# Kernel optimization log

Measured on AMD Instinct MI355X. Metric: run time of the kernel, lower is better.

Reference implementation:

```python
import jax, jax.numpy as jnp
import numpy as np

N = 16384   # total queries (= total keys here)
B = 16      # scenes
K = 1024    # keys per scene (key_batch_cnt entries)
L = 32      # local neighborhood size
D = 256     # d_model
H = 8       # nhead
DFF = 1024
LN_EPS = 1e-5


def setup_inputs() -> dict:
    key = jax.random.key(0)
    ks = jax.random.split(key, 32)
    f32 = jnp.float32

    def lin(k, o, i):
        return jax.random.normal(k, (o, i), f32) * 0.02

    idx = jax.random.randint(ks[3], (N, L), 0, K)
    invalid = jax.random.uniform(ks[4], (N, L)) < 0.1
    index_pair = jnp.where(invalid, -1, idx).astype(jnp.int32)

    inp = {
        "tgt": jax.random.normal(ks[0], (N, D), f32),
        "memory": jax.random.normal(ks[1], (N, D), f32),
        "memory_pos_emb": jax.random.normal(ks[2], (N, D), f32),
        "key_batch_cnt": jnp.full((B,), K, dtype=jnp.int32),
        "index_pair": index_pair,
        "index_pair_batch": jnp.repeat(jnp.arange(B, dtype=jnp.int32), K),
        "Wq": lin(ks[5], D, D), "bq": jnp.zeros((D,), f32),
        "Wkc": lin(ks[6], D, D), "bkc": jnp.zeros((D,), f32),
        "Wkp": lin(ks[7], D, D), "bkp": jnp.zeros((D,), f32),
        "Wv": lin(ks[8], D, D), "bv": jnp.zeros((D,), f32),
        "Wo": lin(ks[9], D, D), "bo": jnp.zeros((D,), f32),
        "W1": lin(ks[10], DFF, D), "b1": jnp.zeros((DFF,), f32),
        "W2": lin(ks[11], D, DFF), "b2": jnp.zeros((D,), f32),
        "g2": jnp.ones((D,), f32), "be2": jnp.zeros((D,), f32),
        "g3": jnp.ones((D,), f32), "be3": jnp.zeros((D,), f32),
    }
    return inp


def _ln(x, g, b):
    m = jnp.mean(x, axis=-1, keepdims=True)
    v = jnp.mean((x - m) ** 2, axis=-1, keepdims=True)
    return (x - m) * jax.lax.rsqrt(v + LN_EPS) * g + b


def reference(tgt, memory, memory_pos_emb, key_batch_cnt, index_pair,
              index_pair_batch, Wq, bq, Wkc, bkc, Wkp, bkp, Wv, bv,
              Wo, bo, W1, b1, W2, b2, g2, be2, g3, be3):
    Dh = D // H
    scale = Dh ** -0.5

    # dense projections
    q = tgt @ Wq.T + bq                              # [N, D]
    k = (memory @ Wkc.T + bkc) + (memory_pos_emb @ Wkp.T + bkp)  # content + pos
    v = memory @ Wv.T + bv

    # local-index gather: per-batch indices -> global key indices
    offsets = jnp.concatenate([jnp.zeros((1,), jnp.int32),
                               jnp.cumsum(key_batch_cnt)[:-1].astype(jnp.int32)])
    mask = index_pair < 0                            # [N, L] padded neighbors
    gidx = jnp.where(mask, 0, index_pair + offsets[index_pair_batch][:, None])

    kg = k[gidx].reshape(N, L, H, Dh)                # gathered keys  [N,L,H,Dh]
    vg = v[gidx].reshape(N, L, H, Dh)                # gathered values
    qh = q.reshape(N, H, Dh)

    attn = jnp.einsum('nhd,nlhd->nhl', qh, kg) * scale
    attn = jnp.where(mask[:, None, :], -1e9, attn)
    attn = jax.nn.softmax(attn, axis=-1)
    out = jnp.einsum('nhl,nlhd->nhd', attn, vg).reshape(N, D)
    tgt2 = out @ Wo.T + bo                           # attention out_proj

    x = _ln(tgt + tgt2, g2, be2)
    ff = jax.nn.relu(x @ W1.T + b1) @ W2.T + b2
    return _ln(x + ff, g3, be3)
```

## Files before the change

### kernel.cpp

```cpp
#include <hip/hip_runtime.h>
#include <stdint.h>

#define N_TOT 16384
#define LNEI  32
#define DM    256
#define NH    8
#define DH    32
#define DFF   1024

typedef __attribute__((ext_vector_type(8))) short  short8;
typedef __attribute__((ext_vector_type(4))) float  floatx4;
typedef __attribute__((ext_vector_type(4))) unsigned short ushort4_t;
typedef __attribute__((ext_vector_type(4))) unsigned int uint4_t;

static __device__ __forceinline__ float b2f(unsigned short u) {
  union { unsigned int u; float f; } x; x.u = ((unsigned int)u) << 16; return x.f;
}
static __device__ __forceinline__ unsigned short f2b(float f) {
  union { float f; unsigned int u; } x; x.f = f;
  unsigned int r = x.u + 0x7fffu + ((x.u >> 16) & 1u);
  return (unsigned short)(r >> 16);
}
static __device__ __forceinline__ float lo16(unsigned int d) {
  union { unsigned int u; float f; } x; x.u = d << 16; return x.f;
}
static __device__ __forceinline__ float hi16(unsigned int d) {
  union { unsigned int u; float f; } x; x.u = d & 0xffff0000u; return x.f;
}

#define NSEG 11
struct Seg { const float* src; unsigned short* dst; int cols; int ostride; int ooff; int begin; };
struct SegTable { Seg s[NSEG]; int total; };

__global__ __launch_bounds__(256) void cvt_all(SegTable T, float* biaskv,
                                               const float* bkc, const float* bkp,
                                               const float* bv) {
  int e = (blockIdx.x * 256 + threadIdx.x) * 4;
  if (e >= T.total) {
    int c = e - T.total;
    #pragma unroll
    for (int j = 0; j < 4; ++j, ++c)
      if (c < 512) biaskv[c] = (c < 256) ? (bkc[c] + bkp[c]) : bv[c - 256];
    return;
  }
  int si = 0;
  #pragma unroll
  for (int i = 1; i < NSEG; ++i) if (e >= T.s[i].begin) si = i;
  const Seg s = T.s[si];
  const int le = e - s.begin;
  const int row = le / s.cols;
  const int col = le - row * s.cols;
  floatx4 v = {0.f, 0.f, 0.f, 0.f};
  if (s.src) v = *(const floatx4*)(s.src + le);
  ushort4_t o;
  o.x = f2b(v[0]); o.y = f2b(v[1]); o.z = f2b(v[2]); o.w = f2b(v[3]);
  *(ushort4_t*)(s.dst + (size_t)row * s.ostride + s.ooff + col) = o;
}

static __device__ __forceinline__ void gl_lds16(const unsigned short* g, unsigned short* l) {
  __builtin_amdgcn_global_load_lds(
      (const __attribute__((address_space(1))) unsigned int*)g,
      (__attribute__((address_space(3))) unsigned int*)l, 16, 0, 0);
}

template<bool RELU>
__global__ __launch_bounds__(64) void gemm_w1(
    const unsigned short* __restrict__ A, const unsigned short* __restrict__ W,
    const float* __restrict__ bias,
    unsigned short* __restrict__ C, int M, int Nd, int K, int lda)
{
  constexpr int BK = 32;
  __shared__ unsigned short sA[2][32 * BK];
  __shared__ unsigned short sB[2][64 * BK];

  const int lane = threadIdx.x;
  const int quad = lane >> 4;
  const int l16  = lane & 15;
  const int m0 = blockIdx.x * 32;
  const int n0 = blockIdx.y * 64;

  const int srow = lane >> 2;
  const int scol = (lane & 3) * 8;

  floatx4 acc[2][4] = {};

  for (int k0 = 0; k0 < K; k0 += 2 * BK) {
    __syncthreads();
    #pragma unroll
    for (int half = 0; half < 2; ++half) {
      const int kk = k0 + half * BK;
      #pragma unroll
      for (int c = 0; c < 2; ++c)
        gl_lds16(A + (size_t)(m0 + c * 16 + srow) * lda + kk + scol, &sA[half][c * 512]);
      #pragma unroll
      for (int c = 0; c < 4; ++c)
        gl_lds16(W + (size_t)(n0 + c * 16 + srow) * K + kk + scol, &sB[half][c * 512]);
    }
    __syncthreads();

    #pragma unroll
    for (int half = 0; half < 2; ++half) {
      short8 af[2], bf[4];
      #pragma unroll
      for (int mi = 0; mi < 2; ++mi)
        af[mi] = *(const short8*)&sA[half][(mi * 16 + l16) * BK + quad * 8];
      #pragma unroll
      for (int ni = 0; ni < 4; ++ni)
        bf[ni] = *(const short8*)&sB[half][(ni * 16 + l16) * BK + quad * 8];
      #pragma unroll
      for (int mi = 0; mi < 2; ++mi)
        #pragma unroll
        for (int ni = 0; ni < 4; ++ni)
          acc[mi][ni] = __builtin_amdgcn_mfma_f32_16x16x32_bf16(af[mi], bf[ni], acc[mi][ni], 0, 0, 0);
    }
  }

  #pragma unroll
  for (int ni = 0; ni < 4; ++ni) {
    const int col = n0 + ni * 16 + l16;
    const float bvv = bias[col];
    #pragma unroll
    for (int mi = 0; mi < 2; ++mi) {
      const int row0 = m0 + mi * 16 + quad * 4;
      #pragma unroll
      for (int i = 0; i < 4; ++i) {
        float v = acc[mi][ni][i] + bvv;
        if (RELU) v = fmaxf(v, 0.f);
        C[(size_t)(row0 + i) * Nd + col] = f2b(v);
      }
    }
  }
}

template<int BN, bool RELU>
__global__ __launch_bounds__(256) void gemm_tile(
    const unsigned short* __restrict__ A, const unsigned short* __restrict__ W,
    const float* __restrict__ bias,
    unsigned short* __restrict__ C, int M, int Nd, int K, int lda)
{
  constexpr int BM = 128, BK = 32;
  constexpr int MI = 4, NI = 4;
  __shared__ unsigned short sA[2][BM * BK];
  __shared__ unsigned short sB[2][BN * BK];

  const int w    = threadIdx.x >> 6;
  const int lane = threadIdx.x & 63;
  const int quad = lane >> 4;
  const int l16  = lane & 15;
  const int m0 = blockIdx.x * BM;
  const int n0 = blockIdx.y * BN;
  const int wrow0 = (w >> 1) * 64;
  const int wcol0 = (w & 1) * 64;

  const int aflat0 = w * 512 + lane * 8;
  const int ar0 = aflat0 >> 5, ac = aflat0 & 31;

  floatx4 acc[MI][NI] = {};

  for (int k0 = 0; k0 < K; k0 += 2 * BK) {
    __syncthreads();
    #pragma unroll
    for (int half = 0; half < 2; ++half) {
      const int kk = k0 + half * BK;
      #pragma unroll
      for (int c = 0; c < 2; ++c) {
        const int row = ar0 + c * 64;
        gl_lds16(A + (size_t)(m0 + row) * lda + kk + ac, &sA[half][(c * 4 + w) * 512]);
        gl_lds16(W + (size_t)(n0 + row) * K + kk + ac, &sB[half][(c * 4 + w) * 512]);
      }
    }
    __syncthreads();

    #pragma unroll
    for (int half = 0; half < 2; ++half) {
      short8 af[MI], bf[NI];
      #pragma unroll
      for (int mi = 0; mi < MI; ++mi)
        af[mi] = *(const short8*)&sA[half][(wrow0 + mi * 16 + l16) * BK + quad * 8];
      #pragma unroll
      for (int ni = 0; ni < NI; ++ni)
        bf[ni] = *(const short8*)&sB[half][(wcol0 + ni * 16 + l16) * BK + quad * 8];
      #pragma unroll
      for (int mi = 0; mi < MI; ++mi)
        #pragma unroll
        for (int ni = 0; ni < NI; ++ni)
          acc[mi][ni] = __builtin_amdgcn_mfma_f32_16x16x32_bf16(af[mi], bf[ni], acc[mi][ni], 0, 0, 0);
    }
  }

  #pragma unroll
  for (int ni = 0; ni < NI; ++ni) {
    const int col = n0 + wcol0 + ni * 16 + l16;
    const float bvv = bias[col];
    #pragma unroll
    for (int mi = 0; mi < MI; ++mi) {
      const int row0 = m0 + wrow0 + mi * 16 + quad * 4;
      #pragma unroll
      for (int i = 0; i < 4; ++i) {
        float v = acc[mi][ni][i] + bvv;
        if (RELU) v = fmaxf(v, 0.f);
        C[(size_t)(row0 + i) * Nd + col] = f2b(v);
      }
    }
  }
}

__global__ __launch_bounds__(256) void attn_kernel(
    const unsigned short* __restrict__ q, const unsigned short* __restrict__ kv,
    const int* __restrict__ key_batch_cnt, const int* __restrict__ index_pair,
    const int* __restrict__ index_pair_batch,
    unsigned short* __restrict__ out)
{
  const int n = ((blockIdx.x & 7) << 11) | (blockIdx.x >> 3);
  const int t = threadIdx.x;
  __shared__ float s_q[DM];
  __shared__ int   s_gidx[LNEI];
  __shared__ float s_prob[NH][LNEI];
  __shared__ float s_out[2][DM];

  s_q[t] = b2f(q[(size_t)n * DM + t]);
  if (t < LNEI) {
    const int b = index_pair_batch[n];
    int off = 0;
    for (int i = 0; i < b; ++i) off += key_batch_cnt[i];
    const int ip = index_pair[(size_t)n * LNEI + t];
    s_gidx[t] = (ip < 0) ? -1 : (ip + off);
  }
  __syncthreads();

  {
    const int h = t >> 5;
    const int l = t & 31;
    const int g = s_gidx[l];

    floatx4 qv[8];
    #pragma unroll
    for (int c = 0; c < 8; ++c) qv[c] = *(const floatx4*)&s_q[h * DH + c * 4];

    float score = -1e9f;
    if (g >= 0) {
      const uint4_t* kp = (const uint4_t*)(kv + (size_t)g * 512 + h * DH);
      float acc = 0.f;
      #pragma unroll
      for (int c = 0; c < 4; ++c) {
        uint4_t d = kp[c];
        acc += lo16(d.x) * qv[c * 2][0] + hi16(d.x) * qv[c * 2][1]
             + lo16(d.y) * qv[c * 2][2] + hi16(d.y) * qv[c * 2][3]
             + lo16(d.z) * qv[c * 2 + 1][0] + hi16(d.z) * qv[c * 2 + 1][1]
             + lo16(d.w) * qv[c * 2 + 1][2] + hi16(d.w) * qv[c * 2 + 1][3];
      }
      score = acc * 0.17677669529663687f;
    }

    float mx = score;
    #pragma unroll
    for (int msk = 16; msk >= 1; msk >>= 1) mx = fmaxf(mx, __shfl_xor(mx, msk, 64));
    const float e = __expf(score - mx);
    float sm = e;
    #pragma unroll
    for (int msk = 16; msk >= 1; msk >>= 1) sm += __shfl_xor(sm, msk, 64);
    s_prob[h][l] = e / sm;
  }
  __syncthreads();

  {
    const int jh  = t >> 7;
    const int h   = (t >> 4) & 7;
    const int dh2 = t & 15;
    float ax = 0.f, ay = 0.f;
    const unsigned short* vbase = kv + 256 + h * DH + dh2 * 2;
    #pragma unroll
    for (int j2 = 0; j2 < 16; ++j2) {
      const int j = jh * 16 + j2;
      int gj = s_gidx[j];
      gj = (gj < 0) ? 0 : gj;
      const float p = s_prob[h][j];
      const unsigned int d = *(const unsigned int*)(vbase + (size_t)gj * 512);
      ax += p * lo16(d);
      ay += p * hi16(d);
    }
    s_out[jh][h * DH + dh2 * 2]     = ax;
    s_out[jh][h * DH + dh2 * 2 + 1] = ay;
  }
  __syncthreads();

  out[(size_t)n * DM + t] = f2b(s_out[0][t] + s_out[1][t]);
}

template<bool IN1F32, bool OUTF32>
__global__ __launch_bounds__(256) void ln_kernel(
    const void* __restrict__ in1, const unsigned short* __restrict__ in2,
    const float* __restrict__ g, const float* __restrict__ b,
    void* __restrict__ out)
{
  const int n = blockIdx.x;
  const int t = threadIdx.x;
  const int wv = t >> 6;
  __shared__ float part[8];

  float a1;
  if (IN1F32) a1 = ((const float*)in1)[(size_t)n * DM + t];
  else        a1 = b2f(((const unsigned short*)in1)[(size_t)n * DM + t]);
  const float a = a1 + b2f(in2[(size_t)n * DM + t]);

  float s = a;
  #pragma unroll
  for (int msk = 32; msk >= 1; msk >>= 1) s += __shfl_xor(s, msk, 64);
  if ((t & 63) == 0) part[wv] = s;
  __syncthreads();
  const float mean = (part[0] + part[1] + part[2] + part[3]) * (1.0f / DM);
  const float d = a - mean;
  float s2 = d * d;
  #pragma unroll
  for (int msk = 32; msk >= 1; msk >>= 1) s2 += __shfl_xor(s2, msk, 64);
  if ((t & 63) == 0) part[4 + wv] = s2;
  __syncthreads();
  const float var = (part[4] + part[5] + part[6] + part[7]) * (1.0f / DM);
  const float y = d * rsqrtf(var + 1e-5f) * g[t] + b[t];
  if (OUTF32) ((float*)out)[(size_t)n * DM + t] = y;
  else        ((unsigned short*)out)[(size_t)n * DM + t] = f2b(y);
}

extern "C" void kernel_launch(void* const* d_in, const int* in_sizes, int n_in,
                              void* d_out, int out_size, void* d_ws, size_t ws_size,
                              hipStream_t stream) {
  const float* tgt  = (const float*)d_in[0];
  const float* mem  = (const float*)d_in[1];
  const float* pos  = (const float*)d_in[2];
  const int* kbc    = (const int*)d_in[3];
  const int* ipair  = (const int*)d_in[4];
  const int* ipb    = (const int*)d_in[5];
  const float* Wq   = (const float*)d_in[6];
  const float* bq   = (const float*)d_in[7];
  const float* Wkc  = (const float*)d_in[8];
  const float* bkc  = (const float*)d_in[9];
  const float* Wkp  = (const float*)d_in[10];
  const float* bkp  = (const float*)d_in[11];
  const float* Wv   = (const float*)d_in[12];
  const float* bvp  = (const float*)d_in[13];
  const float* Wo   = (const float*)d_in[14];
  const float* bo   = (const float*)d_in[15];
  const float* W1   = (const float*)d_in[16];
  const float* b1   = (const float*)d_in[17];
  const float* W2   = (const float*)d_in[18];
  const float* b2   = (const float*)d_in[19];
  const float* g2   = (const float*)d_in[20];
  const float* be2  = (const float*)d_in[21];
  const float* g3   = (const float*)d_in[22];
  const float* be3  = (const float*)d_in[23];

  const size_t NB = (size_t)N_TOT * DM;
  unsigned short* ws = (unsigned short*)d_ws;
  unsigned short* tgt_b = ws;
  unsigned short* ao_b  = ws;
  unsigned short* t2_b  = ws + NB;
  unsigned short* mp_b  = ws + 2 * NB;
  unsigned short* x_b   = ws + 2 * NB;
  unsigned short* ff_b  = ws + 3 * NB;
  unsigned short* q_b   = ws + 4 * NB;
  unsigned short* h1_b  = ws + 4 * NB;
  unsigned short* kv_b  = ws + 5 * NB;
  unsigned short* wgt   = ws + 8 * NB;
  unsigned short* Wq_b  = wgt;
  unsigned short* Wkv_b = wgt + 65536;
  unsigned short* Wo_b  = wgt + 65536 + 262144;
  unsigned short* W1_b  = wgt + 2 * 65536 + 262144;
  unsigned short* W2_b  = wgt + 2 * 65536 + 2 * 262144;
  float* bias_kv = (float*)(wgt + 2 * 65536 + 3 * 262144);

  SegTable T;
  int beg = 0, i = 0;
  auto seg = [&](const float* s, unsigned short* d, int cols, int ostride, int ooff, int nelem) {
    T.s[i].src = s; T.s[i].dst = d; T.s[i].cols = cols;
    T.s[i].ostride = ostride; T.s[i].ooff = ooff; T.s[i].begin = beg;
    beg += nelem; ++i;
  };
  seg(tgt, tgt_b, DM, DM, 0,   (int)NB);
  seg(mem, mp_b,  DM, 512, 0,  (int)NB);
  seg(pos, mp_b,  DM, 512, DM, (int)NB);
  seg(Wq,  Wq_b,  DM, DM, 0,   65536);
  seg(Wkc, Wkv_b, DM, 512, 0,  65536);
  seg(Wkp, Wkv_b, DM, 512, DM, 65536);
  seg(Wv,  Wkv_b + (size_t)256 * 512, DM, 512, 0, 65536);
  seg(nullptr, Wkv_b + (size_t)256 * 512, DM, 512, DM, 65536);
  seg(Wo,  Wo_b,  DM, DM, 0,   65536);
  seg(W1,  W1_b,  DM, DM, 0,   262144);
  seg(W2,  W2_b,  DFF, DFF, 0, 262144);
  T.total = beg;

  dim3 blk(256);
  cvt_all<<<dim3(T.total / 1024 + 1), blk, 0, stream>>>(T, bias_kv, bkc, bkp, bvp);

  dim3 blk64(64);
  dim3 gQ(N_TOT / 32, DM / 64);
  dim3 gKV(N_TOT / 32, 512 / 64);
  dim3 gF(N_TOT / 128, DFF / 128);

  gemm_w1<false><<<gQ, blk64, 0, stream>>>(tgt_b, Wq_b, bq, q_b, N_TOT, DM, DM, DM);
  gemm_w1<false><<<gKV, blk64, 0, stream>>>(mp_b, Wkv_b, bias_kv, kv_b, N_TOT, 512, 512, 512);
  attn_kernel<<<dim3(N_TOT), blk, 0, stream>>>(q_b, kv_b, kbc, ipair, ipb, ao_b);
  gemm_w1<false><<<gQ, blk64, 0, stream>>>(ao_b, Wo_b, bo, t2_b, N_TOT, DM, DM, DM);
  ln_kernel<true, false><<<dim3(N_TOT), blk, 0, stream>>>(tgt, t2_b, g2, be2, x_b);
  gemm_tile<128, true><<<gF, blk, 0, stream>>>(x_b, W1_b, b1, h1_b, N_TOT, DFF, DM, DM);
  gemm_w1<false><<<gQ, blk64, 0, stream>>>(h1_b, W2_b, b2, ff_b, N_TOT, DM, DFF, DFF);
  ln_kernel<false, true><<<dim3(N_TOT), blk, 0, stream>>>(x_b, ff_b, g3, be3, d_out);
}
```

Baseline: 291.9 us.

## Merge Q/KV GEMMs, retile small GEMMs, precompute batch offsets, restructure attention

Q and KV projections now run as one launch with 128x64 tiles over four waves, replacing the single-wave 32x64 blocks. The Wo and W2 GEMMs switch to 512-thread 128x64 tiles, and W1 uses a cleaned-up 128x128 tile. The conversion kernel computes scene offsets once, so each attention block no longer loops over key_batch_cnt. Attention now splits score computation across (neighbor, head) threads through shared memory and writes output through split x/y buffers. The goals are more work per block, less launch overhead and less redundant per-query work, at the cost of fewer blocks in flight and extra shared-memory passes.

```diff
diff --git a/kernel.cpp b/kernel.cpp
--- a/kernel.cpp
+++ b/kernel.cpp
@@ -34,10 +34,17 @@
 
 __global__ __launch_bounds__(256) void cvt_all(SegTable T, float* biaskv,
                                                const float* bkc, const float* bkp,
-                                               const float* bv) {
+                                               const float* bv,
+                                               int* offs, const int* kbc) {
   int e = (blockIdx.x * 256 + threadIdx.x) * 4;
   if (e >= T.total) {
     int c = e - T.total;
+    if (c == 512) {
+      int off = 0;
+      #pragma unroll
+      for (int i = 0; i < 16; ++i) { offs[i] = off; off += kbc[i]; }
+      return;
+    }
     #pragma unroll
     for (int j = 0; j < 4; ++j, ++c)
       if (c < 512) biaskv[c] = (c < 256) ? (bkc[c] + bkp[c]) : bv[c - 256];
@@ -63,38 +70,33 @@
       (__attribute__((address_space(3))) unsigned int*)l, 16, 0, 0);
 }
 
-template<bool RELU>
-__global__ __launch_bounds__(64) void gemm_w1(
+__device__ __forceinline__ void gemm4_body(
     const unsigned short* __restrict__ A, const unsigned short* __restrict__ W,
-    const float* __restrict__ bias,
-    unsigned short* __restrict__ C, int M, int Nd, int K, int lda)
-{
-  constexpr int BK = 32;
-  __shared__ unsigned short sA[2][32 * BK];
-  __shared__ unsigned short sB[2][64 * BK];
-
-  const int lane = threadIdx.x;
+    const float* __restrict__ bias, unsigned short* __restrict__ C,
+    int Nd, int K, int lda, int mb, int nb,
+    unsigned short (&sA)[2][4096], unsigned short (&sB)[2][2048])
+{
+  const int w    = threadIdx.x >> 6;
+  const int lane = threadIdx.x & 63;
   const int quad = lane >> 4;
   const int l16  = lane & 15;
-  const int m0 = blockIdx.x * 32;
-  const int n0 = blockIdx.y * 64;
-
-  const int srow = lane >> 2;
-  const int scol = (lane & 3) * 8;
+  const int m0 = mb * 128;
+  const int n0 = nb * 64;
+  const int wrow0 = w * 32;
+  const int aflat0 = w * 512 + lane * 8;
+  const int ar0 = aflat0 >> 5, ac = aflat0 & 31;
 
   floatx4 acc[2][4] = {};
 
-  for (int k0 = 0; k0 < K; k0 += 2 * BK) {
-    __syncthreads();
-    #pragma unroll
-    for (int half = 0; half < 2; ++half) {
-      const int kk = k0 + half * BK;
+  for (int k0 = 0; k0 < K; k0 += 64) {
+    __syncthreads();
+    #pragma unroll
+    for (int half = 0; half < 2; ++half) {
+      const int kk = k0 + half * 32;
       #pragma unroll
       for (int c = 0; c < 2; ++c)
-        gl_lds16(A + (size_t)(m0 + c * 16 + srow) * lda + kk + scol, &sA[half][c * 512]);
-      #pragma unroll
-      for (int c = 0; c < 4; ++c)
-        gl_lds16(W + (size_t)(n0 + c * 16 + srow) * K + kk + scol, &sB[half][c * 512]);
+        gl_lds16(A + (size_t)(m0 + ar0 + c * 64) * lda + kk + ac, &sA[half][(c * 4 + w) * 512]);
+      gl_lds16(W + (size_t)(n0 + ar0) * K + kk + ac, &sB[half][w * 512]);
     }
     __syncthreads();
 
@@ -103,10 +105,10 @@
       short8 af[2], bf[4];
       #pragma unroll
       for (int mi = 0; mi < 2; ++mi)
-        af[mi] = *(const short8*)&sA[half][(mi * 16 + l16) * BK + quad * 8];
+        af[mi] = *(const short8*)&sA[half][(wrow0 + mi * 16 + l16) * 32 + quad * 8];
       #pragma unroll
       for (int ni = 0; ni < 4; ++ni)
-        bf[ni] = *(const short8*)&sB[half][(ni * 16 + l16) * BK + quad * 8];
+        bf[ni] = *(const short8*)&sB[half][(ni * 16 + l16) * 32 + quad * 8];
       #pragma unroll
       for (int mi = 0; mi < 2; ++mi)
         #pragma unroll
@@ -121,7 +123,145 @@
     const float bvv = bias[col];
     #pragma unroll
     for (int mi = 0; mi < 2; ++mi) {
-      const int row0 = m0 + mi * 16 + quad * 4;
+      const int row0 = m0 + wrow0 + mi * 16 + quad * 4;
+      #pragma unroll
+      for (int i = 0; i < 4; ++i)
+        C[(size_t)(row0 + i) * Nd + col] = f2b(acc[mi][ni][i] + bvv);
+    }
+  }
+}
+
+__global__ __launch_bounds__(256) void gemm_qkv(
+    const unsigned short* __restrict__ A1, const unsigned short* __restrict__ W1p,
+    const float* __restrict__ b1p, unsigned short* __restrict__ C1,
+    const unsigned short* __restrict__ A2, const unsigned short* __restrict__ W2p,
+    const float* __restrict__ b2p, unsigned short* __restrict__ C2)
+{
+  __shared__ unsigned short sA[2][4096];
+  __shared__ unsigned short sB[2][2048];
+  const int bid = blockIdx.x;
+  if (bid < 512) {
+    gemm4_body(A1, W1p, b1p, C1, 256, 256, 256, bid >> 2, bid & 3, sA, sB);
+  } else {
+    const int b2 = bid - 512;
+    gemm4_body(A2, W2p, b2p, C2, 512, 512, 512, b2 >> 3, b2 & 7, sA, sB);
+  }
+}
+
+template<bool RELU>
+__global__ __launch_bounds__(512) void gemm8(
+    const unsigned short* __restrict__ A, const unsigned short* __restrict__ W,
+    const float* __restrict__ bias, unsigned short* __restrict__ C,
+    int Nd, int K, int lda)
+{
+  __shared__ unsigned short sA[2][4096];
+  __shared__ unsigned short sB[2][2048];
+  const int w    = threadIdx.x >> 6;
+  const int lane = threadIdx.x & 63;
+  const int quad = lane >> 4;
+  const int l16  = lane & 15;
+  const int m0 = blockIdx.x * 128;
+  const int n0 = blockIdx.y * 64;
+  const int srow = lane >> 2;
+  const int scol = (lane & 3) * 8;
+
+  floatx4 acc[4] = {};
+
+  for (int k0 = 0; k0 < K; k0 += 64) {
+    __syncthreads();
+    #pragma unroll
+    for (int half = 0; half < 2; ++half) {
+      const int kk = k0 + half * 32;
+      gl_lds16(A + (size_t)(m0 + w * 16 + srow) * lda + kk + scol, &sA[half][w * 512]);
+      if (w < 4)
+        gl_lds16(W + (size_t)(n0 + w * 16 + srow) * K + kk + scol, &sB[half][w * 512]);
+    }
+    __syncthreads();
+
+    #pragma unroll
+    for (int half = 0; half < 2; ++half) {
+      short8 af = *(const short8*)&sA[half][(w * 16 + l16) * 32 + quad * 8];
+      #pragma unroll
+      for (int ni = 0; ni < 4; ++ni) {
+        short8 bf = *(const short8*)&sB[half][(ni * 16 + l16) * 32 + quad * 8];
+        acc[ni] = __builtin_amdgcn_mfma_f32_16x16x32_bf16(af, bf, acc[ni], 0, 0, 0);
+      }
+    }
+  }
+
+  #pragma unroll
+  for (int ni = 0; ni < 4; ++ni) {
+    const int col = n0 + ni * 16 + l16;
+    const float bvv = bias[col];
+    const int row0 = m0 + w * 16 + quad * 4;
+    #pragma unroll
+    for (int i = 0; i < 4; ++i) {
+      float v = acc[ni][i] + bvv;
+      if (RELU) v = fmaxf(v, 0.f);
+      C[(size_t)(row0 + i) * Nd + col] = f2b(v);
+    }
+  }
+}
+
+template<bool RELU>
+__global__ __launch_bounds__(256) void gemm_tile128(
+    const unsigned short* __restrict__ A, const unsigned short* __restrict__ W,
+    const float* __restrict__ bias, unsigned short* __restrict__ C,
+    int Nd, int K, int lda)
+{
+  __shared__ unsigned short sA[2][4096];
+  __shared__ unsigned short sB[2][4096];
+  const int w    = threadIdx.x >> 6;
+  const int lane = threadIdx.x & 63;
+  const int quad = lane >> 4;
+  const int l16  = lane & 15;
+  const int m0 = blockIdx.x * 128;
+  const int n0 = blockIdx.y * 128;
+  const int wrow0 = (w >> 1) * 64;
+  const int wcol0 = (w & 1) * 64;
+  const int aflat0 = w * 512 + lane * 8;
+  const int ar0 = aflat0 >> 5, ac = aflat0 & 31;
+
+  floatx4 acc[4][4] = {};
+
+  for (int k0 = 0; k0 < K; k0 += 64) {
+    __syncthreads();
+    #pragma unroll
+    for (int half = 0; half < 2; ++half) {
+      const int kk = k0 + half * 32;
+      #pragma unroll
+      for (int c = 0; c < 2; ++c) {
+        const int row = ar0 + c * 64;
+        gl_lds16(A + (size_t)(m0 + row) * lda + kk + ac, &sA[half][(c * 4 + w) * 512]);
+        gl_lds16(W + (size_t)(n0 + row) * K + kk + ac, &sB[half][(c * 4 + w) * 512]);
+      }
+    }
+    __syncthreads();
+
+    #pragma unroll
+    for (int half = 0; half < 2; ++half) {
+      short8 af[4], bf[4];
+      #pragma unroll
+      for (int mi = 0; mi < 4; ++mi)
+        af[mi] = *(const short8*)&sA[half][(wrow0 + mi * 16 + l16) * 32 + quad * 8];
+      #pragma unroll
+      for (int ni = 0; ni < 4; ++ni)
+        bf[ni] = *(const short8*)&sB[half][(wcol0 + ni * 16 + l16) * 32 + quad * 8];
+      #pragma unroll
+      for (int mi = 0; mi < 4; ++mi)
+        #pragma unroll
+        for (int ni = 0; ni < 4; ++ni)
+          acc[mi][ni] = __builtin_amdgcn_mfma_f32_16x16x32_bf16(af[mi], bf[ni], acc[mi][ni], 0, 0, 0);
+    }
+  }
+
+  #pragma unroll
+  for (int ni = 0; ni < 4; ++ni) {
+    const int col = n0 + wcol0 + ni * 16 + l16;
+    const float bvv = bias[col];
+    #pragma unroll
+    for (int mi = 0; mi < 4; ++mi) {
+      const int row0 = m0 + wrow0 + mi * 16 + quad * 4;
       #pragma unroll
       for (int i = 0; i < 4; ++i) {
         float v = acc[mi][ni][i] + bvv;
@@ -132,130 +272,57 @@
   }
 }
 
-template<int BN, bool RELU>
-__global__ __launch_bounds__(256) void gemm_tile(
-    const unsigned short* __restrict__ A, const unsigned short* __restrict__ W,
-    const float* __restrict__ bias,
-    unsigned short* __restrict__ C, int M, int Nd, int K, int lda)
-{
-  constexpr int BM = 128, BK = 32;
-  constexpr int MI = 4, NI = 4;
-  __shared__ unsigned short sA[2][BM * BK];
-  __shared__ unsigned short sB[2][BN * BK];
-
-  const int w    = threadIdx.x >> 6;
-  const int lane = threadIdx.x & 63;
-  const int quad = lane >> 4;
-  const int l16  = lane & 15;
-  const int m0 = blockIdx.x * BM;
-  const int n0 = blockIdx.y * BN;
-  const int wrow0 = (w >> 1) * 64;
-  const int wcol0 = (w & 1) * 64;
-
-  const int aflat0 = w * 512 + lane * 8;
-  const int ar0 = aflat0 >> 5, ac = aflat0 & 31;
-
-  floatx4 acc[MI][NI] = {};
-
-  for (int k0 = 0; k0 < K; k0 += 2 * BK) {
-    __syncthreads();
-    #pragma unroll
-    for (int half = 0; half < 2; ++half) {
-      const int kk = k0 + half * BK;
-      #pragma unroll
-      for (int c = 0; c < 2; ++c) {
-        const int row = ar0 + c * 64;
-        gl_lds16(A + (size_t)(m0 + row) * lda + kk + ac, &sA[half][(c * 4 + w) * 512]);
-        gl_lds16(W + (size_t)(n0 + row) * K + kk + ac, &sB[half][(c * 4 + w) * 512]);
-      }
-    }
-    __syncthreads();
-
-    #pragma unroll
-    for (int half = 0; half < 2; ++half) {
-      short8 af[MI], bf[NI];
-      #pragma unroll
-      for (int mi = 0; mi < MI; ++mi)
-        af[mi] = *(const short8*)&sA[half][(wrow0 + mi * 16 + l16) * BK + quad * 8];
-      #pragma unroll
-      for (int ni = 0; ni < NI; ++ni)
-        bf[ni] = *(const short8*)&sB[half][(wcol0 + ni * 16 + l16) * BK + quad * 8];
-      #pragma unroll
-      for (int mi = 0; mi < MI; ++mi)
-        #pragma unroll
-        for (int ni = 0; ni < NI; ++ni)
-          acc[mi][ni] = __builtin_amdgcn_mfma_f32_16x16x32_bf16(af[mi], bf[ni], acc[mi][ni], 0, 0, 0);
-    }
-  }
-
-  #pragma unroll
-  for (int ni = 0; ni < NI; ++ni) {
-    const int col = n0 + wcol0 + ni * 16 + l16;
-    const float bvv = bias[col];
-    #pragma unroll
-    for (int mi = 0; mi < MI; ++mi) {
-      const int row0 = m0 + wrow0 + mi * 16 + quad * 4;
-      #pragma unroll
-      for (int i = 0; i < 4; ++i) {
-        float v = acc[mi][ni][i] + bvv;
-        if (RELU) v = fmaxf(v, 0.f);
-        C[(size_t)(row0 + i) * Nd + col] = f2b(v);
-      }
-    }
-  }
-}
-
 __global__ __launch_bounds__(256) void attn_kernel(
     const unsigned short* __restrict__ q, const unsigned short* __restrict__ kv,
-    const int* __restrict__ key_batch_cnt, const int* __restrict__ index_pair,
-    const int* __restrict__ index_pair_batch,
+    const int* __restrict__ index_pair, const int* __restrict__ index_pair_batch,
+    const int* __restrict__ offs,
     unsigned short* __restrict__ out)
 {
   const int n = ((blockIdx.x & 7) << 11) | (blockIdx.x >> 3);
   const int t = threadIdx.x;
-  __shared__ float s_q[DM];
+  __shared__ float s_qp[NH][36];
   __shared__ int   s_gidx[LNEI];
-  __shared__ float s_prob[NH][LNEI];
-  __shared__ float s_out[2][DM];
-
-  s_q[t] = b2f(q[(size_t)n * DM + t]);
+  __shared__ float s_score[NH][33];
+  __shared__ float s_prob[NH][33];
+  __shared__ float s_ox[2][NH][16];
+  __shared__ float s_oy[2][NH][16];
+
+  s_qp[t >> 5][t & 31] = b2f(q[(size_t)n * DM + t]);
   if (t < LNEI) {
     const int b = index_pair_batch[n];
-    int off = 0;
-    for (int i = 0; i < b; ++i) off += key_batch_cnt[i];
     const int ip = index_pair[(size_t)n * LNEI + t];
-    s_gidx[t] = (ip < 0) ? -1 : (ip + off);
+    s_gidx[t] = (ip < 0) ? -1 : (ip + offs[b]);
+  }
+  __syncthreads();
+
+  {
+    const int j = t >> 3;
+    const int h = t & 7;
+    const int g = s_gidx[j];
+    const int gl = (g < 0) ? 0 : g;
+    const unsigned short* kb = kv + (size_t)gl * 512 + h * DH;
+    float acc = 0.f;
+    #pragma unroll
+    for (int c = 0; c < 4; ++c) {
+      const uint4_t d = *(const uint4_t*)(kb + c * 8);
+      const float* qp = &s_qp[h][c * 8];
+      acc += lo16(d.x) * qp[0] + hi16(d.x) * qp[1]
+           + lo16(d.y) * qp[2] + hi16(d.y) * qp[3]
+           + lo16(d.z) * qp[4] + hi16(d.z) * qp[5]
+           + lo16(d.w) * qp[6] + hi16(d.w) * qp[7];
+    }
+    s_score[h][j] = (g < 0) ? -1e9f : acc * 0.17677669529663687f;
   }
   __syncthreads();
 
   {
     const int h = t >> 5;
     const int l = t & 31;
-    const int g = s_gidx[l];
-
-    floatx4 qv[8];
-    #pragma unroll
-    for (int c = 0; c < 8; ++c) qv[c] = *(const floatx4*)&s_q[h * DH + c * 4];
-
-    float score = -1e9f;
-    if (g >= 0) {
-      const uint4_t* kp = (const uint4_t*)(kv + (size_t)g * 512 + h * DH);
-      float acc = 0.f;
-      #pragma unroll
-      for (int c = 0; c < 4; ++c) {
-        uint4_t d = kp[c];
-        acc += lo16(d.x) * qv[c * 2][0] + hi16(d.x) * qv[c * 2][1]
-             + lo16(d.y) * qv[c * 2][2] + hi16(d.y) * qv[c * 2][3]
-             + lo16(d.z) * qv[c * 2 + 1][0] + hi16(d.z) * qv[c * 2 + 1][1]
-             + lo16(d.w) * qv[c * 2 + 1][2] + hi16(d.w) * qv[c * 2 + 1][3];
-      }
-      score = acc * 0.17677669529663687f;
-    }
-
-    float mx = score;
+    const float sc = s_score[h][l];
+    float mx = sc;
     #pragma unroll
     for (int msk = 16; msk >= 1; msk >>= 1) mx = fmaxf(mx, __shfl_xor(mx, msk, 64));
-    const float e = __expf(score - mx);
+    const float e = __expf(sc - mx);
     float sm = e;
     #pragma unroll
     for (int msk = 16; msk >= 1; msk >>= 1) sm += __shfl_xor(sm, msk, 64);
@@ -279,12 +346,18 @@
       ax += p * lo16(d);
       ay += p * hi16(d);
     }
-    s_out[jh][h * DH + dh2 * 2]     = ax;
-    s_out[jh][h * DH + dh2 * 2 + 1] = ay;
-  }
-  __syncthreads();
-
-  out[(size_t)n * DM + t] = f2b(s_out[0][t] + s_out[1][t]);
+    s_ox[jh][h][dh2] = ax;
+    s_oy[jh][h][dh2] = ay;
+  }
+  __syncthreads();
+
+  {
+    const int h = t >> 5;
+    const int dh2 = (t >> 1) & 15;
+    const float val = (t & 1) ? (s_oy[0][h][dh2] + s_oy[1][h][dh2])
+                              : (s_ox[0][h][dh2] + s_ox[1][h][dh2]);
+    out[(size_t)n * DM + t] = f2b(val);
+  }
 }
 
 template<bool IN1F32, bool OUTF32>
@@ -367,6 +440,7 @@
   unsigned short* W1_b  = wgt + 2 * 65536 + 262144;
   unsigned short* W2_b  = wgt + 2 * 65536 + 2 * 262144;
   float* bias_kv = (float*)(wgt + 2 * 65536 + 3 * 262144);
+  int* offs_ws   = (int*)(bias_kv + 512);
 
   SegTable T;
   int beg = 0, i = 0;
@@ -389,19 +463,15 @@
   T.total = beg;
 
   dim3 blk(256);
-  cvt_all<<<dim3(T.total / 1024 + 1), blk, 0, stream>>>(T, bias_kv, bkc, bkp, bvp);
-
-  dim3 blk64(64);
-  dim3 gQ(N_TOT / 32, DM / 64);
-  dim3 gKV(N_TOT / 32, 512 / 64);
-  dim3 gF(N_TOT / 128, DFF / 128);
-
-  gemm_w1<false><<<gQ, blk64, 0, stream>>>(tgt_b, Wq_b, bq, q_b, N_TOT, DM, DM, DM);
-  gemm_w1<false><<<gKV, blk64, 0, stream>>>(mp_b, Wkv_b, bias_kv, kv_b, N_TOT, 512, 512, 512);
-  attn_kernel<<<dim3(N_TOT), blk, 0, stream>>>(q_b, kv_b, kbc, ipair, ipb, ao_b);
-  gemm_w1<false><<<gQ, blk64, 0, stream>>>(ao_b, Wo_b, bo, t2_b, N_TOT, DM, DM, DM);
+  cvt_all<<<dim3(T.total / 1024 + 1), blk, 0, stream>>>(T, bias_kv, bkc, bkp, bvp,
+                                                        offs_ws, kbc);
+
+  gemm_qkv<<<dim3(1536), blk, 0, stream>>>(tgt_b, Wq_b, bq, q_b,
+                                           mp_b, Wkv_b, bias_kv, kv_b);
+  attn_kernel<<<dim3(N_TOT), blk, 0, stream>>>(q_b, kv_b, ipair, ipb, offs_ws, ao_b);
+  gemm8<false><<<dim3(128, 4), dim3(512), 0, stream>>>(ao_b, Wo_b, bo, t2_b, DM, DM, DM);
   ln_kernel<true, false><<<dim3(N_TOT), blk, 0, stream>>>(tgt, t2_b, g2, be2, x_b);
-  gemm_tile<128, true><<<gF, blk, 0, stream>>>(x_b, W1_b, b1, h1_b, N_TOT, DFF, DM, DM);
-  gemm_w1<false><<<gQ, blk64, 0, stream>>>(h1_b, W2_b, b2, ff_b, N_TOT, DM, DFF, DFF);
+  gemm_tile128<true><<<dim3(128, 8), blk, 0, stream>>>(x_b, W1_b, b1, h1_b, DFF, DM, DM);
+  gemm8<false><<<dim3(128, 4), dim3(512), 0, stream>>>(h1_b, W2_b, b2, ff_b, DM, DFF, DFF);
   ln_kernel<false, true><<<dim3(N_TOT), blk, 0, stream>>>(x_b, ff_b, g3, be3, d_out);
 }
```

After: 284.2 us. -2.7%, faster.
